# Kernel optimization log

Hardware: AMD Instinct MI355X
Metric: run time of the kernel (lower is better)

## Reference

```python
import jax, jax.numpy as jnp
import numpy as np

NUM_CLASSES = 80
LAMBDA_OBJ, LAMBDA_NOOBJ, LAMBDA_BBOX, LAMBDA_CLASS = 1.0, 0.5, 5.0, 1.0
IOU_POS = 0.5
ALPHA, GAMMA = 0.25, 2.0


def setup_inputs() -> dict:
    key = jax.random.key(0)
    ks = jax.random.split(key, 7)
    B, A, H, W, C, M = 8, 3, 80, 80, NUM_CLASSES, 100
    objectness = jax.random.uniform(ks[0], (B, A, H, W, 1), dtype=jnp.float32)
    xy = jax.random.uniform(ks[1], (B, A, H, W, 2), dtype=jnp.float32)
    wh = 0.05 + 0.25 * jax.random.uniform(ks[2], (B, A, H, W, 2), dtype=jnp.float32)
    boxes = jnp.concatenate([xy, wh], axis=-1)  # (cx,cy,w,h)
    class_scores = jax.random.normal(ks[3], (B, A, H, W, C), dtype=jnp.float32)
    txy = jax.random.uniform(ks[4], (B, M, 2), dtype=jnp.float32)
    twh = 0.05 + 0.25 * jax.random.uniform(ks[5], (B, M, 2), dtype=jnp.float32)
    target_boxes = jnp.concatenate([txy, twh], axis=-1)
    target_labels = jax.random.randint(ks[6], (B, M), 0, C)
    return {"objectness": objectness, "boxes": boxes, "class_scores": class_scores,
            "target_boxes": target_boxes, "target_labels": target_labels}


def _box_iou(b1, b2):
    # b1: [N,4], b2: [M,4] in (cx,cy,w,h) -> IoU [N,M]
    b1_lo = b1[:, :2] - b1[:, 2:] * 0.5
    b1_hi = b1[:, :2] + b1[:, 2:] * 0.5
    b2_lo = b2[:, :2] - b2[:, 2:] * 0.5
    b2_hi = b2[:, :2] + b2[:, 2:] * 0.5
    lo = jnp.maximum(b1_lo[:, None, :], b2_lo[None, :, :])
    hi = jnp.minimum(b1_hi[:, None, :], b2_hi[None, :, :])
    wh = jnp.clip(hi - lo, 0.0)
    inter = wh[..., 0] * wh[..., 1]
    a1 = b1[:, 2] * b1[:, 3]
    a2 = b2[:, 2] * b2[:, 3]
    union = a1[:, None] + a2[None, :] - inter
    return inter / (union + 1e-6)


def _giou(b1, b2):
    # elementwise pairs [N,4],[N,4] -> [N]
    b1_lo = b1[:, :2] - b1[:, 2:] * 0.5
    b1_hi = b1[:, :2] + b1[:, 2:] * 0.5
    b2_lo = b2[:, :2] - b2[:, 2:] * 0.5
    b2_hi = b2[:, :2] + b2[:, 2:] * 0.5
    wh = jnp.clip(jnp.minimum(b1_hi, b2_hi) - jnp.maximum(b1_lo, b2_lo), 0.0)
    inter = wh[:, 0] * wh[:, 1]
    union = b1[:, 2] * b1[:, 3] + b2[:, 2] * b2[:, 3] - inter
    iou = inter / (union + 1e-6)
    ewh = jnp.clip(jnp.maximum(b1_hi, b2_hi) - jnp.minimum(b1_lo, b2_lo), 0.0)
    enclose = ewh[:, 0] * ewh[:, 1]
    return iou - (enclose - union) / (enclose + 1e-6)


def _per_image(obj, boxes, cls, tb, tl):
    # obj:[N], boxes:[N,4], cls:[N,C], tb:[M,4], tl:[M]
    N = boxes.shape[0]
    iou = _box_iou(boxes, tb)                 # [N,M] -- dominant intermediate
    max_iou = jnp.max(iou, axis=1)
    idx = jnp.argmax(iou, axis=1)
    pos = max_iou >= IOU_POS
    posf = pos.astype(boxes.dtype)
    bbox_t = tb[idx] * posf[:, None]          # zeros for negatives
    class_t = jnp.where(pos, tl[idx], 0)
    # objectness BCE (torch BCELoss clamps log terms at -100), summed over anchors
    logp = jnp.maximum(jnp.log(obj), -100.0)
    log1mp = jnp.maximum(jnp.log1p(-obj), -100.0)
    bce_sum = -jnp.sum(posf * logp + (1.0 - posf) * log1mp)
    pos_cnt = jnp.sum(posf)
    # faithful to source: scalar BCE sum broadcast over masks then re-summed
    obj_term = bce_sum * (LAMBDA_OBJ * pos_cnt + LAMBDA_NOOBJ * (N - pos_cnt))
    # GIoU bbox loss over positive anchors
    giou = _giou(boxes, bbox_t)
    bbox_sum = jnp.sum((1.0 - giou) * posf)
    # focal loss (logits) vs one-hot, mean over positive subset [P,C]
    onehot = jax.nn.one_hot(class_t, NUM_CLASSES, dtype=cls.dtype)
    p = jax.nn.sigmoid(cls)
    ce = jnp.maximum(cls, 0.0) - cls * onehot + jnp.log1p(jnp.exp(-jnp.abs(cls)))
    p_t = p * onehot + (1.0 - p) * (1.0 - onehot)
    a_t = ALPHA * onehot + (1.0 - ALPHA) * (1.0 - onehot)
    fl = a_t * (1.0 - p_t) ** GAMMA * ce
    class_sum = jnp.sum(fl * posf[:, None]) / jnp.maximum(pos_cnt * NUM_CLASSES, 1.0)
    return obj_term, bbox_sum, class_sum, pos_cnt


def _forward(objectness, boxes, class_scores, target_boxes, target_labels):
    B = objectness.shape[0]
    obj_f = objectness.reshape(B, -1)
    box_f = boxes.reshape(B, -1, 4)
    cls_f = class_scores.reshape(B, -1, NUM_CLASSES)
    o, bb, cl, pc = jax.vmap(_per_image)(obj_f, box_f, cls_f, target_boxes, target_labels)
    num_pos = jnp.maximum(jnp.sum(pc), 1.0)
    obj_loss = jnp.sum(o) / B
    bbox_loss = LAMBDA_BBOX * jnp.sum(bb) / num_pos
    class_loss = LAMBDA_CLASS * jnp.sum(cl) / B
    return obj_loss + bbox_loss + class_loss


def reference(objectness, boxes, class_scores, target_boxes, target_labels):
    return _forward(objectness, boxes, class_scores, target_boxes, target_labels)
```

## Files before the change

kernel.cpp:

```cpp
#include <hip/hip_runtime.h>
#include <math.h>

#define NCLS    80
#define MTGT    100
#define NANCH   19200
#define BATCH   8
#define BLKA    64
#define NBLK    (NANCH / BLKA)
#define NWAVE   4
#define TSLICE  (MTGT / NWAVE)
#define ROW4    (NCLS / 4)

__device__ __forceinline__ float fast_rcp(float x) { return __builtin_amdgcn_rcpf(x); }

__device__ __forceinline__ float focal_term(float x, bool is_t) {
    const float ax  = fabsf(x);
    const float q   = __expf(-ax);
    const float ce0 = fmaxf(x, 0.0f) + __logf(1.0f + q);
    const float r   = fast_rcp(1.0f + q);
    const float p   = (x >= 0.0f) ? r : q * r;
    const float pt  = is_t ? (1.0f - p) : p;
    const float ce  = is_t ? (ce0 - x) : ce0;
    const float at  = is_t ? 0.25f : 0.75f;
    return at * pt * pt * ce;
}

__global__ __launch_bounds__(256) void anchor_kernel(
    const float* __restrict__ obj, const float* __restrict__ boxes,
    const float* __restrict__ cls, const float* __restrict__ tb,
    const int* __restrict__ tl, float4* __restrict__ partials)
{
    __shared__ float4 t_box[MTGT];
    __shared__ float  t_area[MTGT];
    __shared__ int    t_lab[MTGT];
    __shared__ float  m_bi[NWAVE][BLKA];
    __shared__ float  m_bu[NWAVE][BLKA];
    __shared__ int    m_ix[NWAVE][BLKA];
    __shared__ float  s_posf[BLKA];
    __shared__ int    s_lab[BLKA];
    __shared__ float  s_foc[NWAVE];
    __shared__ float  s_bpb[3];

    const int b    = blockIdx.y;
    const int tid  = threadIdx.x;
    const int wave = tid >> 6;
    const int lane = tid & 63;

    if (tid < MTGT) {
        const float4 t = ((const float4*)tb)[b * MTGT + tid];
        t_box[tid]  = make_float4(t.x - 0.5f * t.z, t.y - 0.5f * t.w,
                                  t.x + 0.5f * t.z, t.y + 0.5f * t.w);
        t_area[tid] = t.z * t.w;
        t_lab[tid]  = tl[b * MTGT + tid];
    }
    __syncthreads();

    const int a0  = blockIdx.x * BLKA;
    const int gid = b * NANCH + a0 + lane;

    const float4 bx = ((const float4*)boxes)[gid];
    const float lox = bx.x - 0.5f * bx.z, loy = bx.y - 0.5f * bx.w;
    const float hix = bx.x + 0.5f * bx.z, hiy = bx.y + 0.5f * bx.w;
    const float a1  = bx.z * bx.w;
    const float aa  = a1 + 1e-6f;

    float bi = -1.0f, bu = 1.0f; int bidx = 0;
    const int m0 = wave * TSLICE;
    #pragma unroll
    for (int mm = 0; mm < TSLICE; ++mm) {
        const int m = m0 + mm;
        const float4 t = t_box[m];
        float iw = fmaxf(fminf(hix, t.z) - fmaxf(lox, t.x), 0.0f);
        float ih = fmaxf(fminf(hiy, t.w) - fmaxf(loy, t.y), 0.0f);
        float inter = iw * ih;
        float uni   = aa + t_area[m] - inter;
        if (inter * bu > bi * uni) { bi = inter; bu = uni; bidx = m; }
    }
    m_bi[wave][lane] = bi;
    m_bu[wave][lane] = bu;
    m_ix[wave][lane] = bidx;
    __syncthreads();

    if (wave == 0) {
        float Bi = m_bi[0][lane], Bu = m_bu[0][lane]; int Bx = m_ix[0][lane];
        #pragma unroll
        for (int w = 1; w < NWAVE; ++w) {
            const float ci = m_bi[w][lane], cu = m_bu[w][lane];
            if (ci * Bu > Bi * cu) { Bi = ci; Bu = cu; Bx = m_ix[w][lane]; }
        }

        const bool  pos  = (Bi + Bi >= Bu);
        const float posf = pos ? 1.0f : 0.0f;
        s_posf[lane] = posf;
        s_lab[lane]  = t_lab[Bx];

        const float o   = obj[gid];
        const float bce = -fmaxf(__logf(pos ? o : 1.0f - o), -100.0f);

        float bbox_l = 0.0f;
        if (pos) {
            const float4 t   = t_box[Bx];
            const float uni  = a1 + t_area[Bx] - Bi;
            const float iou  = Bi * fast_rcp(Bu);
            const float ew   = fmaxf(fmaxf(hix, t.z) - fminf(lox, t.x), 0.0f);
            const float eh   = fmaxf(fmaxf(hiy, t.w) - fminf(loy, t.y), 0.0f);
            const float enc  = ew * eh;
            const float giou = iou - (enc - uni) * fast_rcp(enc + 1e-6f);
            bbox_l = 1.0f - giou;
        }

        float v0 = bce, v1 = posf, v2 = bbox_l;
        #pragma unroll
        for (int off = 32; off; off >>= 1) {
            v0 += __shfl_down(v0, off);
            v1 += __shfl_down(v1, off);
            v2 += __shfl_down(v2, off);
        }
        if (lane == 0) { s_bpb[0] = v0; s_bpb[1] = v1; s_bpb[2] = v2; }
    }
    __syncthreads();

    float focal = 0.0f;
    #pragma unroll
    for (int k = 0; k < 5; ++k) {
        const int flat = k * 256 + tid;
        const int a    = flat / ROW4;
        const int j4   = flat - a * ROW4;
        const float pf = s_posf[a];
        if (pf != 0.0f) {
            const int c = s_lab[a];
            const float4 v = *(const float4*)(cls +
                ((long)(b * NANCH + a0 + a)) * NCLS + j4 * 4);
            float f = focal_term(v.x, 4 * j4 + 0 == c)
                    + focal_term(v.y, 4 * j4 + 1 == c)
                    + focal_term(v.z, 4 * j4 + 2 == c)
                    + focal_term(v.w, 4 * j4 + 3 == c);
            focal += f;
        }
    }
    #pragma unroll
    for (int off = 32; off; off >>= 1)
        focal += __shfl_down(focal, off);
    if (lane == 0) s_foc[wave] = focal;
    __syncthreads();

    if (tid == 0) {
        const float fsum = s_foc[0] + s_foc[1] + s_foc[2] + s_foc[3];
        partials[b * NBLK + blockIdx.x] =
            make_float4(s_bpb[0], s_bpb[1], s_bpb[2], fsum);
    }
}

__global__ __launch_bounds__(512) void finalize_kernel(
    const float4* __restrict__ partials, float* __restrict__ out)
{
    const int wave = threadIdx.x >> 6;
    const int lane = threadIdx.x & 63;

    float s0 = 0.f, s1 = 0.f, s2 = 0.f, s3 = 0.f;
    for (int blk = lane; blk < NBLK; blk += 64) {
        const float4 p = partials[wave * NBLK + blk];
        s0 += p.x; s1 += p.y; s2 += p.z; s3 += p.w;
    }
    #pragma unroll
    for (int off = 32; off; off >>= 1) {
        s0 += __shfl_down(s0, off);
        s1 += __shfl_down(s1, off);
        s2 += __shfl_down(s2, off);
        s3 += __shfl_down(s3, off);
    }
    __shared__ float img[BATCH][4];
    if (lane == 0) { img[wave][0] = s0; img[wave][1] = s1; img[wave][2] = s2; img[wave][3] = s3; }
    __syncthreads();
    if (threadIdx.x == 0) {
        float sum_pc = 0.f, obj_l = 0.f, bbox_s = 0.f, cls_l = 0.f;
        #pragma unroll
        for (int b = 0; b < BATCH; ++b) {
            const float bce = img[b][0];
            const float pc  = img[b][1];
            const float bb  = img[b][2];
            const float fo  = img[b][3];
            sum_pc += pc;
            obj_l  += bce * (1.0f * pc + 0.5f * ((float)NANCH - pc));
            bbox_s += bb;
            cls_l  += fo / fmaxf(pc * (float)NCLS, 1.0f);
        }
        const float num_pos = fmaxf(sum_pc, 1.0f);
        out[0] = obj_l / (float)BATCH + 5.0f * bbox_s / num_pos + cls_l / (float)BATCH;
    }
}

extern "C" void kernel_launch(void* const* d_in, const int* in_sizes, int n_in,
                              void* d_out, int out_size, void* d_ws, size_t ws_size,
                              hipStream_t stream) {
    const float* obj   = (const float*)d_in[0];
    const float* boxes = (const float*)d_in[1];
    const float* cls   = (const float*)d_in[2];
    const float* tb    = (const float*)d_in[3];
    const int*   tl    = (const int*)d_in[4];
    float* out = (float*)d_out;

    float4* partials = (float4*)d_ws;

    dim3 gridA(NBLK, BATCH);
    anchor_kernel<<<gridA, 256, 0, stream>>>(obj, boxes, cls, tb, tl, partials);
    finalize_kernel<<<1, 512, 0, stream>>>(partials, out);
}
```

Before: 109.5 us.

## Precompute target corners in prep kernel and read them from global in IoU loop

Adds a small prep kernel that converts target boxes to corner form and areas once per batch and stores them in workspace. The IoU loop now reads targets directly from global memory (uniform, cache-resident loads) instead of LDS, and the __syncthreads before the loop is removed. Shared copies are still filled for the later wave-0 and focal phases, which now rely on the later barriers for ordering. This trades one extra kernel launch and global/scalar loads for removing an early barrier and LDS reads.

Result: slower. 112.9 us (+3.1%).

```diff
diff --git a/kernel.cpp b/kernel.cpp
--- a/kernel.cpp
+++ b/kernel.cpp
@@ -25,10 +25,23 @@
     return at * pt * pt * ce;
 }
 
+__global__ __launch_bounds__(256) void prep_kernel(
+    const float* __restrict__ tb, float4* __restrict__ tbx, float* __restrict__ tarea)
+{
+    const int idx = blockIdx.x * 256 + threadIdx.x;
+    if (idx < BATCH * MTGT) {
+        const float4 t = ((const float4*)tb)[idx];
+        tbx[idx]   = make_float4(t.x - 0.5f * t.z, t.y - 0.5f * t.w,
+                                 t.x + 0.5f * t.z, t.y + 0.5f * t.w);
+        tarea[idx] = t.z * t.w;
+    }
+}
+
 __global__ __launch_bounds__(256) void anchor_kernel(
     const float* __restrict__ obj, const float* __restrict__ boxes,
-    const float* __restrict__ cls, const float* __restrict__ tb,
-    const int* __restrict__ tl, float4* __restrict__ partials)
+    const float* __restrict__ cls, const float4* __restrict__ tbx,
+    const float* __restrict__ tarea, const int* __restrict__ tl,
+    float4* __restrict__ partials)
 {
     __shared__ float4 t_box[MTGT];
     __shared__ float  t_area[MTGT];
@@ -47,13 +60,11 @@
     const int lane = tid & 63;
 
     if (tid < MTGT) {
-        const float4 t = ((const float4*)tb)[b * MTGT + tid];
-        t_box[tid]  = make_float4(t.x - 0.5f * t.z, t.y - 0.5f * t.w,
-                                  t.x + 0.5f * t.z, t.y + 0.5f * t.w);
-        t_area[tid] = t.z * t.w;
-        t_lab[tid]  = tl[b * MTGT + tid];
-    }
-    __syncthreads();
+        const int g = b * MTGT + tid;
+        t_box[tid]  = tbx[g];
+        t_area[tid] = tarea[g];
+        t_lab[tid]  = tl[g];
+    }
 
     const int a0  = blockIdx.x * BLKA;
     const int gid = b * NANCH + a0 + lane;
@@ -65,16 +76,17 @@
     const float aa  = a1 + 1e-6f;
 
     float bi = -1.0f, bu = 1.0f; int bidx = 0;
-    const int m0 = wave * TSLICE;
-    #pragma unroll
+    const int m0    = wave * TSLICE;
+    const int mbase = b * MTGT + m0;
+    #pragma unroll 5
     for (int mm = 0; mm < TSLICE; ++mm) {
-        const int m = m0 + mm;
-        const float4 t = t_box[m];
+        const float4 t  = tbx[mbase + mm];
+        const float  ar = tarea[mbase + mm];
         float iw = fmaxf(fminf(hix, t.z) - fmaxf(lox, t.x), 0.0f);
         float ih = fmaxf(fminf(hiy, t.w) - fmaxf(loy, t.y), 0.0f);
         float inter = iw * ih;
-        float uni   = aa + t_area[m] - inter;
-        if (inter * bu > bi * uni) { bi = inter; bu = uni; bidx = m; }
+        float uni   = aa + ar - inter;
+        if (inter * bu > bi * uni) { bi = inter; bu = uni; bidx = m0 + mm; }
     }
     m_bi[wave][lane] = bi;
     m_bu[wave][lane] = bu;
@@ -131,11 +143,10 @@
             const int c = s_lab[a];
             const float4 v = *(const float4*)(cls +
                 ((long)(b * NANCH + a0 + a)) * NCLS + j4 * 4);
-            float f = focal_term(v.x, 4 * j4 + 0 == c)
-                    + focal_term(v.y, 4 * j4 + 1 == c)
-                    + focal_term(v.z, 4 * j4 + 2 == c)
-                    + focal_term(v.w, 4 * j4 + 3 == c);
-            focal += f;
+            focal += focal_term(v.x, 4 * j4 + 0 == c)
+                   + focal_term(v.y, 4 * j4 + 1 == c)
+                   + focal_term(v.z, 4 * j4 + 2 == c)
+                   + focal_term(v.w, 4 * j4 + 3 == c);
         }
     }
     #pragma unroll
@@ -201,8 +212,11 @@
     float* out = (float*)d_out;
 
     float4* partials = (float4*)d_ws;
-
+    float4* tbx      = (float4*)((char*)d_ws + 38400);
+    float*  tarea    = (float*)((char*)d_ws + 38400 + 12800);
+
+    prep_kernel<<<(BATCH * MTGT + 255) / 256, 256, 0, stream>>>(tb, tbx, tarea);
     dim3 gridA(NBLK, BATCH);
-    anchor_kernel<<<gridA, 256, 0, stream>>>(obj, boxes, cls, tb, tl, partials);
+    anchor_kernel<<<gridA, 256, 0, stream>>>(obj, boxes, cls, tbx, tarea, tl, partials);
     finalize_kernel<<<1, 512, 0, stream>>>(partials, out);
 }
```

## Fuse finalize into anchor kernel via last-block atomic counter

Applied to the files above, without the earlier changes.

Removes the separate finalize kernel launch. Each block now bumps a global atomic counter after writing its partial, and the last block to finish reduces all partials and writes the final loss. A hipMemsetAsync resets the counter on every call, so a memset node replaces the second kernel launch. The IoU loop unroll is also reduced from full to 5, which trades ILP for lower register pressure.

New measurement: 156.3 us. +42.8%, slower.

```diff
diff --git a/kernel.cpp b/kernel.cpp
--- a/kernel.cpp
+++ b/kernel.cpp
@@ -10,6 +10,7 @@
 #define NWAVE   4
 #define TSLICE  (MTGT / NWAVE)
 #define ROW4    (NCLS / 4)
+#define NPART   (NBLK * BATCH)
 
 __device__ __forceinline__ float fast_rcp(float x) { return __builtin_amdgcn_rcpf(x); }
 
@@ -28,7 +29,8 @@
 __global__ __launch_bounds__(256) void anchor_kernel(
     const float* __restrict__ obj, const float* __restrict__ boxes,
     const float* __restrict__ cls, const float* __restrict__ tb,
-    const int* __restrict__ tl, float4* __restrict__ partials)
+    const int* __restrict__ tl, float4* __restrict__ partials,
+    unsigned int* __restrict__ counter, float* __restrict__ out)
 {
     __shared__ float4 t_box[MTGT];
     __shared__ float  t_area[MTGT];
@@ -40,6 +42,8 @@
     __shared__ int    s_lab[BLKA];
     __shared__ float  s_foc[NWAVE];
     __shared__ float  s_bpb[3];
+    __shared__ float  s_img[BATCH][4];
+    __shared__ bool   s_last;
 
     const int b    = blockIdx.y;
     const int tid  = threadIdx.x;
@@ -66,7 +70,7 @@
 
     float bi = -1.0f, bu = 1.0f; int bidx = 0;
     const int m0 = wave * TSLICE;
-    #pragma unroll
+    #pragma unroll 5
     for (int mm = 0; mm < TSLICE; ++mm) {
         const int m = m0 + mm;
         const float4 t = t_box[m];
@@ -131,11 +135,10 @@
             const int c = s_lab[a];
             const float4 v = *(const float4*)(cls +
                 ((long)(b * NANCH + a0 + a)) * NCLS + j4 * 4);
-            float f = focal_term(v.x, 4 * j4 + 0 == c)
-                    + focal_term(v.y, 4 * j4 + 1 == c)
-                    + focal_term(v.z, 4 * j4 + 2 == c)
-                    + focal_term(v.w, 4 * j4 + 3 == c);
-            focal += f;
+            focal += focal_term(v.x, 4 * j4 + 0 == c)
+                   + focal_term(v.y, 4 * j4 + 1 == c)
+                   + focal_term(v.z, 4 * j4 + 2 == c)
+                   + focal_term(v.w, 4 * j4 + 3 == c);
         }
     }
     #pragma unroll
@@ -145,41 +148,45 @@
     __syncthreads();
 
     if (tid == 0) {
-        const float fsum = s_foc[0] + s_foc[1] + s_foc[2] + s_foc[3];
         partials[b * NBLK + blockIdx.x] =
-            make_float4(s_bpb[0], s_bpb[1], s_bpb[2], fsum);
-    }
-}
-
-__global__ __launch_bounds__(512) void finalize_kernel(
-    const float4* __restrict__ partials, float* __restrict__ out)
-{
-    const int wave = threadIdx.x >> 6;
-    const int lane = threadIdx.x & 63;
-
-    float s0 = 0.f, s1 = 0.f, s2 = 0.f, s3 = 0.f;
-    for (int blk = lane; blk < NBLK; blk += 64) {
-        const float4 p = partials[wave * NBLK + blk];
-        s0 += p.x; s1 += p.y; s2 += p.z; s3 += p.w;
-    }
+            make_float4(s_bpb[0], s_bpb[1], s_bpb[2],
+                        s_foc[0] + s_foc[1] + s_foc[2] + s_foc[3]);
+        __threadfence();
+        const unsigned old = atomicAdd(counter, 1u);
+        s_last = (old == (unsigned)(NPART - 1));
+    }
+    __syncthreads();
+    if (!s_last) return;
+
+    __threadfence();
     #pragma unroll
-    for (int off = 32; off; off >>= 1) {
-        s0 += __shfl_down(s0, off);
-        s1 += __shfl_down(s1, off);
-        s2 += __shfl_down(s2, off);
-        s3 += __shfl_down(s3, off);
-    }
-    __shared__ float img[BATCH][4];
-    if (lane == 0) { img[wave][0] = s0; img[wave][1] = s1; img[wave][2] = s2; img[wave][3] = s3; }
-    __syncthreads();
-    if (threadIdx.x == 0) {
+    for (int im = wave * 2; im < wave * 2 + 2; ++im) {
+        float s0 = 0.f, s1 = 0.f, s2 = 0.f, s3 = 0.f;
+        for (int blk = lane; blk < NBLK; blk += 64) {
+            const float4 p = partials[im * NBLK + blk];
+            s0 += p.x; s1 += p.y; s2 += p.z; s3 += p.w;
+        }
+        #pragma unroll
+        for (int off = 32; off; off >>= 1) {
+            s0 += __shfl_down(s0, off);
+            s1 += __shfl_down(s1, off);
+            s2 += __shfl_down(s2, off);
+            s3 += __shfl_down(s3, off);
+        }
+        if (lane == 0) {
+            s_img[im][0] = s0; s_img[im][1] = s1;
+            s_img[im][2] = s2; s_img[im][3] = s3;
+        }
+    }
+    __syncthreads();
+    if (tid == 0) {
         float sum_pc = 0.f, obj_l = 0.f, bbox_s = 0.f, cls_l = 0.f;
         #pragma unroll
-        for (int b = 0; b < BATCH; ++b) {
-            const float bce = img[b][0];
-            const float pc  = img[b][1];
-            const float bb  = img[b][2];
-            const float fo  = img[b][3];
+        for (int ib = 0; ib < BATCH; ++ib) {
+            const float bce = s_img[ib][0];
+            const float pc  = s_img[ib][1];
+            const float bb  = s_img[ib][2];
+            const float fo  = s_img[ib][3];
             sum_pc += pc;
             obj_l  += bce * (1.0f * pc + 0.5f * ((float)NANCH - pc));
             bbox_s += bb;
@@ -200,9 +207,12 @@
     const int*   tl    = (const int*)d_in[4];
     float* out = (float*)d_out;
 
-    float4* partials = (float4*)d_ws;
+    float4*       partials = (float4*)d_ws;
+    unsigned int* counter  = (unsigned int*)((char*)d_ws + NPART * 16);
+
+    hipMemsetAsync(counter, 0, 4, stream);
 
     dim3 gridA(NBLK, BATCH);
-    anchor_kernel<<<gridA, 256, 0, stream>>>(obj, boxes, cls, tb, tl, partials);
-    finalize_kernel<<<1, 512, 0, stream>>>(partials, out);
+    anchor_kernel<<<gridA, 256, 0, stream>>>(obj, boxes, cls, tb, tl,
+                                             partials, counter, out);
 }
```
